# Kernel tuning notes

Measured on AMD Instinct MI355X. Metric: run time of the kernel, lower is better.

Reference implementation:

```python
import jax, jax.numpy as jnp
import numpy as np

IN_CH = 512; OUT_CH = 512; NOISE_SIZE = 512; K = 3; A = 0.2
B = 4; H = 32
_G = float(np.sqrt(2.0 / (1.0 + A * A)))                 # leaky_relu gain, a=0.2
CONV_SCALE = _G / float(np.sqrt(IN_CH * K * K))          # equal-lr kaiming scale (fan_in = in_ch*3*3)
MS_SCALE = float(np.sqrt(2.0 / (NOISE_SIZE + IN_CH)))    # equal-lr xavier scale on make_s linear
RGB_SCALE = _G * float(np.sqrt(2.0 / (OUT_CH + 3)))      # equal-lr xavier scale on 1x1 to_rgb


def upsample2x(x):
    # torch F.interpolate(scale_factor=2, mode='bilinear', align_corners=False)
    b, c, h, w = x.shape
    return jax.image.resize(x, (b, c, 2 * h, 2 * w), method='bilinear')


def mod_conv(x, style, weight, bias, ms_w, ms_b, w_scale, demodulate, pad):
    # style -> per-sample input-channel scales s: (B, Cin)
    s = style @ (ms_w.T * MS_SCALE) + ms_b
    Wmod = (weight * w_scale)[None] * s[:, None, :, None, None]   # (B, Cout, Cin, k, k)
    if demodulate:
        d = jax.lax.rsqrt(jnp.sum(Wmod * Wmod, axis=(2, 3, 4)) + 1e-8)
        Wmod = Wmod * d[:, :, None, None, None]
    conv1 = lambda xi, wi: jax.lax.conv_general_dilated(
        xi[None], wi, (1, 1), [(pad, pad), (pad, pad)],
        dimension_numbers=('NCHW', 'OIHW', 'NCHW'))[0]
    y = jax.vmap(conv1)(x, Wmod)                                   # per-sample weights == grouped conv
    return y + bias[None, :, None, None]


def lrelu(x):
    return jnp.where(x >= 0, x, A * x)


def setup_inputs() -> dict:
    key = jax.random.key(0)
    ks = jax.random.split(key, 19)
    r = lambda i, shape: jax.random.normal(ks[i], shape, dtype=jnp.float32)
    return {
        'maps': r(0, (B, IN_CH, H, H)),
        'w': r(1, (B, NOISE_SIZE)),
        'rgb': r(2, (B, 3, H, H)),
        'noise0': r(3, (B, 1, 2 * H, 2 * H)),
        'noise1': r(4, (B, 1, 2 * H, 2 * H)),
        'conv0_w': r(5, (OUT_CH, IN_CH, K, K)),
        'conv0_b': 0.1 * r(6, (OUT_CH,)),
        'ms0_w': r(7, (IN_CH, NOISE_SIZE)),
        'ms0_b': jnp.ones((IN_CH,), jnp.float32),
        'ns0': 0.1 * r(8, (OUT_CH,)),
        'conv1_w': r(9, (OUT_CH, OUT_CH, K, K)),
        'conv1_b': 0.1 * r(10, (OUT_CH,)),
        'ms1_w': r(11, (OUT_CH, NOISE_SIZE)),
        'ms1_b': jnp.ones((OUT_CH,), jnp.float32),
        'ns1': 0.1 * r(12, (OUT_CH,)),
        'rgb_w': r(13, (3, OUT_CH, 1, 1)),
        'rgb_b': 0.1 * r(14, (3,)),
        'msr_w': r(15, (OUT_CH, NOISE_SIZE)),
        'msr_b': jnp.ones((OUT_CH,), jnp.float32),
    }


def reference(maps, w, rgb, noise0, noise1,
              conv0_w, conv0_b, ms0_w, ms0_b, ns0,
              conv1_w, conv1_b, ms1_w, ms1_b, ns1,
              rgb_w, rgb_b, msr_w, msr_b):
    # upsample branch (upsample=True)
    rgb = upsample2x(rgb)
    maps = upsample2x(maps)
    # layer 0: modulated conv -> noise -> leaky relu
    h = mod_conv(maps, w, conv0_w, conv0_b, ms0_w, ms0_b, CONV_SCALE, True, 1)
    h = lrelu(h + ns0[None, :, None, None] * noise0)
    # layer 1
    h = mod_conv(h, w, conv1_w, conv1_b, ms1_w, ms1_b, CONV_SCALE, True, 1)
    h = lrelu(h + ns1[None, :, None, None] * noise1)
    # to_rgb: 1x1 modulated conv, no demodulation
    rgb_out = rgb + mod_conv(h, w, rgb_w, rgb_b, msr_w, msr_b, RGB_SCALE, False, 0)
    return (rgb_out, h)
```

## Files before the change

### kernel.cpp

```cpp
#include <hip/hip_runtime.h>
#include <stdint.h>


#define BATCH 4
#define CH 512
#define NPP 4356
#define HOUT_OFF 49152

static constexpr double G_GAIN = 1.3867504905630728;
static constexpr float CONV_SCALE_F = (float)(G_GAIN / 67.88225099390857);
static constexpr float MS_SCALE_F = 0.044194173824159216f;
static constexpr float RGB_SCALE_F = (float)(G_GAIN * 1.4142135623730951 / 22.693611435820433);

typedef __attribute__((ext_vector_type(8))) short short8;
typedef __attribute__((ext_vector_type(4))) float floatx4;

#define OFF_S0     256
#define OFF_S1     (OFF_S0 + 8192)
#define OFF_SR     (OFF_S1 + 8192)
#define OFF_D0     (OFF_SR + 8192)
#define OFF_D1     (OFF_D0 + 8192)
#define OFF_B0F    (OFF_D1 + 8192)
#define OFF_B1F    (OFF_B0F + 2048)
#define OFF_NS0F   (OFF_B1F + 2048)
#define OFF_NS1F   (OFF_NS0F + 2048)
#define OFF_N0F    (OFF_NS1F + 2048)
#define OFF_N1F    (OFF_N0F + 65536)
#define OFF_WT0    (OFF_N1F + 65536)
#define WT_BYTES   4718592
#define OFF_WT1    (OFF_WT0 + WT_BYTES)
#define OFF_XP0    (OFF_WT1 + WT_BYTES)
#define XP_BYTES   17842176
#define OFF_XP1    (OFF_XP0 + XP_BYTES)

__device__ __forceinline__ float bf2f(unsigned short u) {
  return __uint_as_float(((unsigned int)u) << 16);
}
__device__ __forceinline__ unsigned short f2bf(float f) {
  unsigned int x = __float_as_uint(f);
  unsigned int r = x + 0x7FFFu + ((x >> 16) & 1u);
  return (unsigned short)(r >> 16);
}
__device__ __forceinline__ float ldin(const void* p, long i, int bf) {
  if (bf) return bf2f(((const unsigned short*)p)[i]);
  return ((const float*)p)[i];
}
__device__ __forceinline__ int bfflag_of(const void* msb) {
  return ((const unsigned int*)msb)[0] == 0x3F803F80u ? 1 : 0;
}
__device__ __forceinline__ void async_ld16(const void* g, void* l) {
  __builtin_amdgcn_global_load_lds(
      (const __attribute__((address_space(1))) unsigned int*)g,
      (__attribute__((address_space(3))) unsigned int*)l, 16, 0, 0);
}
__device__ __forceinline__ void upw(int o, int n_in, int& lo, int& hi, float& wlo) {
  int k = o >> 1;
  if (o & 1) { lo = k; hi = k + 1; if (hi > n_in - 1) hi = n_in - 1; wlo = 0.75f; }
  else       { lo = k - 1; if (lo < 0) lo = 0; hi = k; wlo = 0.25f; }
}

__global__ void k_pre(const void* w, const void* msw0, const void* msb0,
                      const void* msw1, const void* msb1,
                      const void* mswr, const void* msbr,
                      const void* b0, const void* b1, const void* nv0,
                      const void* nv1, const void* noise0, const void* noise1,
                      float* s0, float* s1, float* sr,
                      float* ob0, float* ob1, float* ons0, float* ons1,
                      float* on0, float* on1, unsigned short* Xp) {
  const int bf = bfflag_of(msb0);
  const int bid = blockIdx.x;
  if (bid < 264) {
    const int idx = bid * 256 + threadIdx.x;
    const int plane = idx / 132;
    const int rem = idx - plane * 132;
    const int row65 = rem >= 66;
    const int col = rem - (row65 ? 66 : 0);
    const short8 z = {0, 0, 0, 0, 0, 0, 0, 0};
    *(short8*)&Xp[((long)plane * NPP + (row65 ? 65 : 0) * 66 + col) * 8] = z;
    return;
  }
  if (bid < 648) {
    const int b2 = bid - 264;
    const int mat = b2 >> 7, chunk = b2 & 127;
    const int wv = threadIdx.x >> 6, lane = threadIdx.x & 63;
    const int i = chunk * 4 + wv;
    const void* msw; const void* msb; float* out;
    if (mat == 0)      { msw = msw0; msb = msb0; out = s0; }
    else if (mat == 1) { msw = msw1; msb = msb1; out = s1; }
    else               { msw = mswr; msb = msbr; out = sr; }
    float a[4] = {0.f, 0.f, 0.f, 0.f};
    const int n0 = lane * 8;
    if (bf) {
      short8 m8 = *(const short8*)((const unsigned short*)msw + (long)i * 512 + n0);
      for (int b = 0; b < 4; ++b) {
        short8 w8 = *(const short8*)((const unsigned short*)w + b * 512 + n0);
        float s = 0.f;
        for (int e = 0; e < 8; ++e)
          s += bf2f((unsigned short)m8[e]) * bf2f((unsigned short)w8[e]);
        a[b] = s;
      }
    } else {
      const float* mrow = (const float*)msw + (long)i * 512 + n0;
      float4 m0v = *(const float4*)mrow, m1v = *(const float4*)(mrow + 4);
      for (int b = 0; b < 4; ++b) {
        const float* wr = (const float*)w + b * 512 + n0;
        float4 w0v = *(const float4*)wr, w1v = *(const float4*)(wr + 4);
        a[b] = m0v.x * w0v.x + m0v.y * w0v.y + m0v.z * w0v.z + m0v.w * w0v.w +
               m1v.x * w1v.x + m1v.y * w1v.y + m1v.z * w1v.z + m1v.w * w1v.w;
      }
    }
    for (int off = 1; off < 64; off <<= 1)
      for (int b = 0; b < 4; ++b) a[b] += __shfl_xor(a[b], off, 64);
    if (lane == 0) {
      const float mb = ldin(msb, i, bf);
      for (int b = 0; b < 4; ++b) out[b * 512 + i] = a[b] * MS_SCALE_F + mb;
    }
    return;
  }
  const int t = (bid - 648) * 256 + threadIdx.x;
  if (t < 512) {
    ob0[t] = ldin(b0, t, bf); ob1[t] = ldin(b1, t, bf);
    ons0[t] = ldin(nv0, t, bf); ons1[t] = ldin(nv1, t, bf);
  }
  on0[t] = ldin(noise0, t, bf);
  on1[t] = ldin(noise1, t, bf);
}

__global__ void k_wtd(const void* w0, const void* w1, const float* s0, const float* s1,
                      unsigned short* Wt0, unsigned short* Wt1,
                      float* S0, float* S1, const void* msb) {
  const int bf = bfflag_of(msb);
  const int l = blockIdx.x >> 9, co = blockIdx.x & 511;
  const void* w = l ? w1 : w0;
  const float* s = l ? s1 : s0;
  unsigned short* Wt = l ? Wt1 : Wt0;
  float* S = l ? S1 : S0;
  float part[4] = {0.f, 0.f, 0.f, 0.f};
  for (int h = 0; h < 2; ++h) {
    const int ci = threadIdx.x + h * 256;
    const int kb = ci >> 5, q = (ci >> 3) & 3, j = ci & 7;
    const long rbase = ((long)co * 512 + ci) * 9;
    float wsq = 0.f;
    for (int t = 0; t < 9; ++t) {
      float v = ldin(w, rbase + t, bf);
      wsq += v * v;
      Wt[((((long)t * 16 + kb) * 4 + q) * 512 + co) * 8 + j] = f2bf(v);
    }
    for (int b = 0; b < 4; ++b) {
      float sv = s[b * 512 + ci];
      part[b] += sv * sv * wsq;
    }
  }
  __shared__ float red[256 * 4];
  for (int b = 0; b < 4; ++b) red[threadIdx.x * 4 + b] = part[b];
  __syncthreads();
  for (int off = 128; off > 0; off >>= 1) {
    if (threadIdx.x < off)
      for (int b = 0; b < 4; ++b)
        red[threadIdx.x * 4 + b] += red[(threadIdx.x + off) * 4 + b];
    __syncthreads();
  }
  if (threadIdx.x < 4) S[threadIdx.x * 512 + co] = red[threadIdx.x];
}

__global__ void k_upt(const void* maps, const float* s0, unsigned short* Xp0,
                      const void* msb) {
  const int bf = bfflag_of(msb);
  const int t = blockIdx.x, kb = blockIdx.y, b = blockIdx.z;
  __shared__ float lds[32][4][32];
  {
    const int ciq = threadIdx.x >> 5;
    const int x = threadIdx.x & 31;
    for (int cc = 0; cc < 4; ++cc) {
      const int ci = cc * 8 + ciq;
      const long cbase = ((long)(b * 512 + kb * 32 + ci)) << 10;
      for (int r = 0; r < 4; ++r) {
        int ir = 2 * t - 1 + r;
        ir = ir < 0 ? 0 : (ir > 31 ? 31 : ir);
        lds[ci][r][x] = ldin(maps, cbase + ir * 32 + x, bf);
      }
    }
  }
  __syncthreads();
  const int q = threadIdx.x >> 6, px = threadIdx.x & 63;
  int xlo, xhi; float wx;
  upw(px, 32, xlo, xhi, wx);
  float sv[8];
  for (int jj = 0; jj < 8; ++jj) sv[jj] = s0[b * 512 + kb * 32 + q * 8 + jj];
  for (int y = 0; y < 4; ++y) {
    const int yg = 4 * t + y;
    int ylo, yhi; float wy;
    upw(yg, 32, ylo, yhi, wy);
    const int rlo = ylo - (2 * t - 1), rhi = yhi - (2 * t - 1);
    short8 pk;
    for (int jj = 0; jj < 8; ++jj) {
      const int ci = q * 8 + jj;
      float vlo = wx * lds[ci][rlo][xlo] + (1.f - wx) * lds[ci][rlo][xhi];
      float vhi = wx * lds[ci][rhi][xlo] + (1.f - wx) * lds[ci][rhi][xhi];
      float v = (wy * vlo + (1.f - wy) * vhi) * sv[jj];
      pk[jj] = (short)f2bf(v);
    }
    *(short8*)&Xp0[((((long)b * 16 + kb) * 4 + q) * NPP + (yg + 1) * 66 + (px + 1)) * 8] = pk;
  }
}

#define MFMA16 __builtin_amdgcn_mfma_f32_16x16x32_bf16
template <int LAYER>
__global__ __launch_bounds__(256, 2) void k_conv(
    const unsigned short* __restrict__ Wt,
    const unsigned short* Xp,
    const float* __restrict__ Ssum,
    const float* __restrict__ bias,
    const float* __restrict__ nsc,
    const float* __restrict__ noise,
    const float* __restrict__ snext,
    unsigned short* XpOut,
    void* dout,
    const void* __restrict__ msb) {
  __shared__ __align__(16) unsigned short AB[32768];
  const int idx = blockIdx.x;
  const int mt = idx & 3, b = (idx >> 2) & 3, nt = idx >> 4;
  const int m0 = mt << 7, y0 = nt << 1;
  const int lane = threadIdx.x & 63, wv = threadIdx.x >> 6;
  const int wm = wv >> 1, wn = wv & 1;
  const int q = lane >> 4, l15 = lane & 15;

  const floatx4 vz = {0.f, 0.f, 0.f, 0.f};
  floatx4 c00 = vz, c01 = vz, c02 = vz, c03 = vz;
  floatx4 c10 = vz, c11 = vz, c12 = vz, c13 = vz;
  floatx4 c20 = vz, c21 = vz, c22 = vz, c23 = vz;
  floatx4 c30 = vz, c31 = vz, c32 = vz, c33 = vz;

  const int vA = (q << 10) + (wm << 9) + (l15 << 3);
  const int BB = 24576;
  const int vB   = BB + (q << 9) + (l15 << 3);
  const int vBm1 = BB + (q << 9) + ((l15 == 0 ? 0 : l15 - 1) << 3);
  const int vBp1 = BB + (q << 9) + ((l15 == 15 ? 15 : l15 + 1) << 3);
  const bool e0 = (l15 == 0), e15 = (l15 == 15);
  const int c6 = wv * 6;

  auto issueB2 = [&](int kb, int r0) {
    for (int r = 0; r < 2; ++r) {
      const int row = r0 + r;
      const unsigned short* src =
          Xp + ((((long)b * 16 + kb) * 4 + wv) * NPP + (long)(y0 + row) * 66 + 1 + lane) * 8;
      async_ld16(src, &AB[BB + ((row * 4 + wv) << 9)]);
    }
  };
  auto issueA = [&](int kb, int ky, int par) {
#pragma unroll
    for (int k = 0; k < 6; ++k) {
      const int c = c6 + k;
      const int half = c & 1, chunk = c >> 1;
      const int kx = chunk >> 2, qq = chunk & 3;
      const unsigned short* src =
          Wt + ((long)(((ky * 3 + kx) * 16 + kb) * 4 + qq) << 12) +
          ((m0 + half * 64 + lane) << 3);
      async_ld16(src, &AB[par * 12288 + chunk * 1024 + half * 512]);
    }
  };

  const short8 z8 = {0, 0, 0, 0, 0, 0, 0, 0};

#define RND(KY, PA, KB, NKB, NKY, NPA, DOB, DKB, DR0)                          \
  {                                                                            \
    __syncthreads();                                                           \
    issueA((NKB), (NKY), (NPA));                                               \
    if (DOB) issueB2((DKB), (DR0));                                            \
    const int ab = (PA) * 12288 + vA;                                          \
    short8 a00 = *(const short8*)&AB[ab];                                      \
    short8 a01 = *(const short8*)&AB[ab + 128];                                \
    short8 a02 = *(const short8*)&AB[ab + 256];                                \
    short8 a03 = *(const short8*)&AB[ab + 384];                                \
    short8 a10 = *(const short8*)&AB[ab + 4096];                               \
    short8 a11 = *(const short8*)&AB[ab + 4224];                               \
    short8 a12 = *(const short8*)&AB[ab + 4352];                               \
    short8 a13 = *(const short8*)&AB[ab + 4480];                               \
    short8 a20 = *(const short8*)&AB[ab + 8192];                               \
    short8 a21 = *(const short8*)&AB[ab + 8320];                               \
    short8 a22 = *(const short8*)&AB[ab + 8448];                               \
    short8 a23 = *(const short8*)&AB[ab + 8576];                               \
    const int bo = ((wn + (KY)) << 11);                                        \
    {                                                              \
      short8 b0 = *(const short8*)&AB[vBm1 + bo];                              \
      short8 b1 = *(const short8*)&AB[vB + bo + 120];                          \
      short8 b2 = *(const short8*)&AB[vB + bo + 248];                          \
      short8 b3 = *(const short8*)&AB[vB + bo + 376];                          \
      b0 = e0 ? z8 : b0;                                                       \
      c00 = MFMA16(a00, b0, c00, 0, 0, 0); c01 = MFMA16(a00, b1, c01, 0, 0, 0);\
      c02 = MFMA16(a00, b2, c02, 0, 0, 0); c03 = MFMA16(a00, b3, c03, 0, 0, 0);\
      c10 = MFMA16(a01, b0, c10, 0, 0, 0); c11 = MFMA16(a01, b1, c11, 0, 0, 0);\
      c12 = MFMA16(a01, b2, c12, 0, 0, 0); c13 = MFMA16(a01, b3, c13, 0, 0, 0);\
      c20 = MFMA16(a02, b0, c20, 0, 0, 0); c21 = MFMA16(a02, b1, c21, 0, 0, 0);\
      c22 = MFMA16(a02, b2, c22, 0, 0, 0); c23 = MFMA16(a02, b3, c23, 0, 0, 0);\
      c30 = MFMA16(a03, b0, c30, 0, 0, 0); c31 = MFMA16(a03, b1, c31, 0, 0, 0);\
      c32 = MFMA16(a03, b2, c32, 0, 0, 0); c33 = MFMA16(a03, b3, c33, 0, 0, 0);\
    }                                                                          \
    {                                                              \
      short8 b0 = *(const short8*)&AB[vB + bo];                                \
      short8 b1 = *(const short8*)&AB[vB + bo + 128];                          \
      short8 b2 = *(const short8*)&AB[vB + bo + 256];                          \
      short8 b3 = *(const short8*)&AB[vB + bo + 384];                          \
      c00 = MFMA16(a10, b0, c00, 0, 0, 0); c01 = MFMA16(a10, b1, c01, 0, 0, 0);\
      c02 = MFMA16(a10, b2, c02, 0, 0, 0); c03 = MFMA16(a10, b3, c03, 0, 0, 0);\
      c10 = MFMA16(a11, b0, c10, 0, 0, 0); c11 = MFMA16(a11, b1, c11, 0, 0, 0);\
      c12 = MFMA16(a11, b2, c12, 0, 0, 0); c13 = MFMA16(a11, b3, c13, 0, 0, 0);\
      c20 = MFMA16(a12, b0, c20, 0, 0, 0); c21 = MFMA16(a12, b1, c21, 0, 0, 0);\
      c22 = MFMA16(a12, b2, c22, 0, 0, 0); c23 = MFMA16(a12, b3, c23, 0, 0, 0);\
      c30 = MFMA16(a13, b0, c30, 0, 0, 0); c31 = MFMA16(a13, b1, c31, 0, 0, 0);\
      c32 = MFMA16(a13, b2, c32, 0, 0, 0); c33 = MFMA16(a13, b3, c33, 0, 0, 0);\
    }                                                                          \
    {                                                              \
      short8 b0 = *(const short8*)&AB[vB + bo + 8];                            \
      short8 b1 = *(const short8*)&AB[vB + bo + 136];                          \
      short8 b2 = *(const short8*)&AB[vB + bo + 264];                          \
      short8 b3 = *(const short8*)&AB[vBp1 + bo + 384];                        \
      b3 = e15 ? z8 : b3;                                                      \
      c00 = MFMA16(a20, b0, c00, 0, 0, 0); c01 = MFMA16(a20, b1, c01, 0, 0, 0);\
      c02 = MFMA16(a20, b2, c02, 0, 0, 0); c03 = MFMA16(a20, b3, c03, 0, 0, 0);\
      c10 = MFMA16(a21, b0, c10, 0, 0, 0); c11 = MFMA16(a21, b1, c11, 0, 0, 0);\
      c12 = MFMA16(a21, b2, c12, 0, 0, 0); c13 = MFMA16(a21, b3, c13, 0, 0, 0);\
      c20 = MFMA16(a22, b0, c20, 0, 0, 0); c21 = MFMA16(a22, b1, c21, 0, 0, 0);\
      c22 = MFMA16(a22, b2, c22, 0, 0, 0); c23 = MFMA16(a22, b3, c23, 0, 0, 0);\
      c30 = MFMA16(a23, b0, c30, 0, 0, 0); c31 = MFMA16(a23, b1, c31, 0, 0, 0);\
      c32 = MFMA16(a23, b2, c32, 0, 0, 0); c33 = MFMA16(a23, b3, c33, 0, 0, 0);\
    }                                                                          \
  }

  issueA(0, 0, 0);
  issueB2(0, 0);

#pragma unroll 1
  for (int it = 0; it < 8; ++it) {
    const int kb = it * 2, kb1 = kb + 1, kb2 = (kb + 2) & 15;
    RND(0, 0, kb,  kb,  1, 1, 1, kb,  2)
    RND(1, 1, kb,  kb,  2, 0, 0, 0,  0)
    RND(2, 0, kb,  kb1, 0, 1, 1, kb1, 0)
    RND(0, 1, kb1, kb1, 1, 0, 1, kb1, 2)
    RND(1, 0, kb1, kb1, 2, 1, 0, 0,  0)
    RND(2, 1, kb1, kb2, 0, 0, 1, kb2, 0)
  }
#undef RND

  floatx4 accv[4][4] = {{c00, c01, c02, c03}, {c10, c11, c12, c13},
                        {c20, c21, c22, c23}, {c30, c31, c32, c33}};
  const int bfflag = bfflag_of(msb);
  const int coB = m0 + (wm << 6) + ((lane >> 4) << 2);
  const int xB = lane & 15;
  const int y = y0 + wn;
  for (int i = 0; i < 4; ++i) {
    const int co = coB + (i << 4);
    float Ds[4], bi[4], nv[4], sx[4];
    for (int r = 0; r < 4; ++r) {
      float Sv = Ssum[b * 512 + co + r];
      Ds[r] = CONV_SCALE_F * rsqrtf(CONV_SCALE_F * CONV_SCALE_F * Sv + 1e-8f);
      bi[r] = bias[co + r];
      nv[r] = nsc[co + r];
      sx[r] = (LAYER == 0) ? snext[b * 512 + co + r] : 0.f;
    }
    for (int j = 0; j < 4; ++j) {
      const int x = (j << 4) + xB;
      const int p = (y << 6) + x;
      const float nz = noise[b * 4096 + p];
      if (LAYER == 0) {
        unsigned long long pk = 0ull;
        for (int r = 0; r < 4; ++r) {
          float v = accv[i][j][r] * Ds[r] + bi[r] + nv[r] * nz;
          v = (v >= 0.f) ? v : 0.2f * v;
          pk |= (unsigned long long)f2bf(v * sx[r]) << (16 * r);
        }
        const int pp = (y + 1) * 66 + (x + 1);
        const long o = ((((long)b * 16 + (co >> 5)) * 4 + ((co >> 3) & 3)) * NPP + pp) * 8 + (co & 7);
        *(unsigned long long*)(XpOut + o) = pk;
      } else {
        for (int r = 0; r < 4; ++r) {
          float v = accv[i][j][r] * Ds[r] + bi[r] + nv[r] * nz;
          v = (v >= 0.f) ? v : 0.2f * v;
          const long o = (((long)(b * 512 + co + r)) << 12) + p;
          if (bfflag) ((unsigned short*)dout)[HOUT_OFF + o] = f2bf(v);
          else        ((float*)dout)[HOUT_OFF + o] = v;
        }
      }
    }
  }
}

__global__ void k_rgb(const void* rgb_in, const void* rw, const void* rb,
                      const float* sr, void* dout, const void* msb) {
  const int bf = bfflag_of(msb);
  const int b = blockIdx.y, p0 = blockIdx.x * 64;
  const int px = threadIdx.x & 63, g = threadIdx.x >> 6;
  const char* hbytes = (const char*)dout + (long)HOUT_OFF * (bf ? 2 : 4);
  const float* srb = sr + b * 512;
  float a0 = 0.f, a1 = 0.f, a2 = 0.f;
  for (int ci = g * 128; ci < g * 128 + 128; ++ci) {
    const long o = (((long)(b * 512 + ci)) << 12) + p0 + px;
    const float hv = bf ? bf2f(((const unsigned short*)hbytes)[o])
                        : ((const float*)hbytes)[o];
    const float sh = srb[ci] * hv;
    a0 += RGB_SCALE_F * ldin(rw, ci, bf) * sh;
    a1 += RGB_SCALE_F * ldin(rw, 512 + ci, bf) * sh;
    a2 += RGB_SCALE_F * ldin(rw, 1024 + ci, bf) * sh;
  }
  __shared__ float red[4][3][64];
  red[g][0][px] = a0; red[g][1][px] = a1; red[g][2][px] = a2;
  __syncthreads();
  if (g == 0) {
    const int p = p0 + px;
    const int y = p >> 6, x = p & 63;
    int ylo, yhi, xlo, xhi; float wy, wx;
    upw(y, 32, ylo, yhi, wy);
    upw(x, 32, xlo, xhi, wx);
    for (int c = 0; c < 3; ++c) {
      float s = red[0][c][px] + red[1][c][px] + red[2][c][px] + red[3][c][px];
      const long base = (long)(b * 3 + c) << 10;
      const float v00 = ldin(rgb_in, base + ylo * 32 + xlo, bf);
      const float v01 = ldin(rgb_in, base + ylo * 32 + xhi, bf);
      const float v10 = ldin(rgb_in, base + yhi * 32 + xlo, bf);
      const float v11 = ldin(rgb_in, base + yhi * 32 + xhi, bf);
      const float up = wy * (wx * v00 + (1.f - wx) * v01) +
                       (1.f - wy) * (wx * v10 + (1.f - wx) * v11);
      const float v = up + s + ldin(rb, c, bf);
      const long o = ((long)(b * 3 + c) << 12) + p;
      if (bf) ((unsigned short*)dout)[o] = f2bf(v);
      else    ((float*)dout)[o] = v;
    }
  }
}

extern "C" void kernel_launch(void* const* d_in, const int* in_sizes, int n_in,
                              void* d_out, int out_size, void* d_ws, size_t ws_size,
                              hipStream_t stream) {
  char* ws = (char*)d_ws;
  float* s0 = (float*)(ws + OFF_S0);
  float* s1 = (float*)(ws + OFF_S1);
  float* sr = (float*)(ws + OFF_SR);
  float* S0 = (float*)(ws + OFF_D0);
  float* S1 = (float*)(ws + OFF_D1);
  float* b0f = (float*)(ws + OFF_B0F);
  float* b1f = (float*)(ws + OFF_B1F);
  float* ns0f = (float*)(ws + OFF_NS0F);
  float* ns1f = (float*)(ws + OFF_NS1F);
  float* n0f = (float*)(ws + OFF_N0F);
  float* n1f = (float*)(ws + OFF_N1F);
  unsigned short* Wt0 = (unsigned short*)(ws + OFF_WT0);
  unsigned short* Wt1 = (unsigned short*)(ws + OFF_WT1);
  unsigned short* Xp0 = (unsigned short*)(ws + OFF_XP0);
  unsigned short* Xp1 = (unsigned short*)(ws + OFF_XP1);

  k_pre<<<712, 256, 0, stream>>>(d_in[1], d_in[7], d_in[8], d_in[12], d_in[13],
                                 d_in[17], d_in[18], d_in[6], d_in[11], d_in[9],
                                 d_in[14], d_in[3], d_in[4],
                                 s0, s1, sr, b0f, b1f, ns0f, ns1f, n0f, n1f, Xp0);
  k_wtd<<<1024, 256, 0, stream>>>(d_in[5], d_in[10], s0, s1, Wt0, Wt1, S0, S1,
                                  d_in[8]);
  k_upt<<<dim3(16, 16, 4), 256, 0, stream>>>(d_in[0], s0, Xp0, d_in[8]);
  k_conv<0><<<512, 256, 0, stream>>>(Wt0, Xp0, S0, b0f, ns0f, n0f, s1, Xp1,
                                     d_out, d_in[8]);
  k_conv<1><<<512, 256, 0, stream>>>(Wt1, Xp1, S1, b1f, ns1f, n1f, s1, Xp1,
                                     d_out, d_in[8]);
  k_rgb<<<dim3(64, 4), 256, 0, stream>>>(d_in[2], d_in[15], d_in[16], sr, d_out,
                                         d_in[8]);
  (void)in_sizes; (void)n_in; (void)out_size; (void)ws_size;
}
```

Measured before the change: 305.0 us.

## Fuse weight-transform and upsample kernels, vectorize weight prep, precompute to_rgb weights

Merges the weight transpose/demod-sum kernel and the upsample kernel into a single launch, which also precomputes the modulated to_rgb weights. The weight path now has each thread load 72 contiguous weights with vector loads, write packed short8 rows and reduce with wave shuffles instead of an LDS tree. k_rgb processes 8 pixels per thread with vector loads and reads the precomputed modulated weights. This cuts launch count and uncoalesced scalar traffic, but leaves k_rgb with only 32 blocks, which may underfill the GPU.

```diff
diff --git a/kernel.cpp b/kernel.cpp
--- a/kernel.cpp
+++ b/kernel.cpp
@@ -24,7 +24,8 @@
 #define OFF_B1F    (OFF_B0F + 2048)
 #define OFF_NS0F   (OFF_B1F + 2048)
 #define OFF_NS1F   (OFF_NS0F + 2048)
-#define OFF_N0F    (OFF_NS1F + 2048)
+#define OFF_WMODR  (OFF_NS1F + 2048)
+#define OFF_N0F    (OFF_WMODR + 24576)
 #define OFF_N1F    (OFF_N0F + 65536)
 #define OFF_WT0    (OFF_N1F + 65536)
 #define WT_BYTES   4718592
@@ -126,82 +127,131 @@
   on1[t] = ldin(noise1, t, bf);
 }
 
-__global__ void k_wtd(const void* w0, const void* w1, const float* s0, const float* s1,
-                      unsigned short* Wt0, unsigned short* Wt1,
-                      float* S0, float* S1, const void* msb) {
+__global__ void k_mid(const void* w0, const void* w1,
+                      const float* s0, const float* s1, const float* sr,
+                      const void* rw, unsigned short* Wt0, unsigned short* Wt1,
+                      float* S0, float* S1, float* owmr,
+                      const void* maps, unsigned short* Xp0, const void* msb) {
   const int bf = bfflag_of(msb);
-  const int l = blockIdx.x >> 9, co = blockIdx.x & 511;
-  const void* w = l ? w1 : w0;
-  const float* s = l ? s1 : s0;
-  unsigned short* Wt = l ? Wt1 : Wt0;
-  float* S = l ? S1 : S0;
-  float part[4] = {0.f, 0.f, 0.f, 0.f};
-  for (int h = 0; h < 2; ++h) {
-    const int ci = threadIdx.x + h * 256;
-    const int kb = ci >> 5, q = (ci >> 3) & 3, j = ci & 7;
-    const long rbase = ((long)co * 512 + ci) * 9;
-    float wsq = 0.f;
+  const int bid = blockIdx.x;
+  __shared__ float smem[32 * 4 * 32];
+  if (bid < 256) {
+    const int l = bid >> 7, cog = bid & 127;
+    const void* w = l ? w1 : w0;
+    const float* s = l ? s1 : s0;
+    unsigned short* Wt = l ? Wt1 : Wt0;
+    float* S = l ? S1 : S0;
+    const int co_sub = threadIdx.x >> 6;
+    const int kb = (threadIdx.x >> 2) & 15, q = threadIdx.x & 3;
+    const int co = cog * 4 + co_sub;
+    const int ci0 = kb * 32 + q * 8;
+    const long base = ((long)co * 512 + ci0) * 9;
+    float v[9][8];
+    if (bf) {
+      const unsigned short* wp = (const unsigned short*)w + base;
+      short8 r[9];
+#pragma unroll
+      for (int k = 0; k < 9; ++k) r[k] = *(const short8*)(wp + k * 8);
+#pragma unroll
+      for (int j = 0; j < 8; ++j)
+#pragma unroll
+        for (int t = 0; t < 9; ++t) {
+          const int off = j * 9 + t;
+          v[t][j] = bf2f((unsigned short)r[off >> 3][off & 7]);
+        }
+    } else {
+      const float* wp = (const float*)w + base;
+      float4 r[18];
+#pragma unroll
+      for (int k = 0; k < 18; ++k) r[k] = *(const float4*)(wp + k * 4);
+#pragma unroll
+      for (int j = 0; j < 8; ++j)
+#pragma unroll
+        for (int t = 0; t < 9; ++t) {
+          const int off = j * 9 + t;
+          const float4 rr = r[off >> 2];
+          const int c2 = off & 3;
+          v[t][j] = c2 == 0 ? rr.x : (c2 == 1 ? rr.y : (c2 == 2 ? rr.z : rr.w));
+        }
+    }
+#pragma unroll
     for (int t = 0; t < 9; ++t) {
-      float v = ldin(w, rbase + t, bf);
-      wsq += v * v;
-      Wt[((((long)t * 16 + kb) * 4 + q) * 512 + co) * 8 + j] = f2bf(v);
-    }
-    for (int b = 0; b < 4; ++b) {
-      float sv = s[b * 512 + ci];
-      part[b] += sv * sv * wsq;
-    }
-  }
-  __shared__ float red[256 * 4];
-  for (int b = 0; b < 4; ++b) red[threadIdx.x * 4 + b] = part[b];
-  __syncthreads();
-  for (int off = 128; off > 0; off >>= 1) {
-    if (threadIdx.x < off)
-      for (int b = 0; b < 4; ++b)
-        red[threadIdx.x * 4 + b] += red[(threadIdx.x + off) * 4 + b];
+      short8 pk;
+#pragma unroll
+      for (int j = 0; j < 8; ++j) pk[j] = (short)f2bf(v[t][j]);
+      *(short8*)&Wt[((long)(t * 16 + kb) * 4 + q) * 4096 + co * 8] = pk;
+    }
+    float wsq[8];
+#pragma unroll
+    for (int j = 0; j < 8; ++j) {
+      float a = 0.f;
+#pragma unroll
+      for (int t = 0; t < 9; ++t) a += v[t][j] * v[t][j];
+      wsq[j] = a;
+    }
+    float part[4];
+#pragma unroll
+    for (int b4 = 0; b4 < 4; ++b4) {
+      const float* sp = s + b4 * 512 + ci0;
+      float4 sa = *(const float4*)sp, sb = *(const float4*)(sp + 4);
+      part[b4] = sa.x * sa.x * wsq[0] + sa.y * sa.y * wsq[1] +
+                 sa.z * sa.z * wsq[2] + sa.w * sa.w * wsq[3] +
+                 sb.x * sb.x * wsq[4] + sb.y * sb.y * wsq[5] +
+                 sb.z * sb.z * wsq[6] + sb.w * sb.w * wsq[7];
+    }
+    for (int off = 1; off < 64; off <<= 1)
+#pragma unroll
+      for (int b4 = 0; b4 < 4; ++b4)
+        part[b4] += __shfl_xor(part[b4], off, 64);
+    if ((threadIdx.x & 63) == 0)
+#pragma unroll
+      for (int b4 = 0; b4 < 4; ++b4) S[b4 * 512 + co] = part[b4];
+    return;
+  }
+  if (bid < 1280) {
+    const int bid2 = bid - 256;
+    const int t = bid2 & 15, kb = (bid2 >> 4) & 15, b = bid2 >> 8;
+    float (*lds)[4][32] = (float(*)[4][32])smem;
+    {
+      const int ciq = threadIdx.x >> 5;
+      const int x = threadIdx.x & 31;
+      for (int cc = 0; cc < 4; ++cc) {
+        const int ci = cc * 8 + ciq;
+        const long cbase = ((long)(b * 512 + kb * 32 + ci)) << 10;
+        for (int r = 0; r < 4; ++r) {
+          int ir = 2 * t - 1 + r;
+          ir = ir < 0 ? 0 : (ir > 31 ? 31 : ir);
+          lds[ci][r][x] = ldin(maps, cbase + ir * 32 + x, bf);
+        }
+      }
+    }
     __syncthreads();
-  }
-  if (threadIdx.x < 4) S[threadIdx.x * 512 + co] = red[threadIdx.x];
-}
-
-__global__ void k_upt(const void* maps, const float* s0, unsigned short* Xp0,
-                      const void* msb) {
-  const int bf = bfflag_of(msb);
-  const int t = blockIdx.x, kb = blockIdx.y, b = blockIdx.z;
-  __shared__ float lds[32][4][32];
-  {
-    const int ciq = threadIdx.x >> 5;
-    const int x = threadIdx.x & 31;
-    for (int cc = 0; cc < 4; ++cc) {
-      const int ci = cc * 8 + ciq;
-      const long cbase = ((long)(b * 512 + kb * 32 + ci)) << 10;
-      for (int r = 0; r < 4; ++r) {
-        int ir = 2 * t - 1 + r;
-        ir = ir < 0 ? 0 : (ir > 31 ? 31 : ir);
-        lds[ci][r][x] = ldin(maps, cbase + ir * 32 + x, bf);
+    const int q = threadIdx.x >> 6, px = threadIdx.x & 63;
+    int xlo, xhi; float wx;
+    upw(px, 32, xlo, xhi, wx);
+    float sv[8];
+    for (int jj = 0; jj < 8; ++jj) sv[jj] = s0[b * 512 + kb * 32 + q * 8 + jj];
+    for (int y = 0; y < 4; ++y) {
+      const int yg = 4 * t + y;
+      int ylo, yhi; float wy;
+      upw(yg, 32, ylo, yhi, wy);
+      const int rlo = ylo - (2 * t - 1), rhi = yhi - (2 * t - 1);
+      short8 pk;
+      for (int jj = 0; jj < 8; ++jj) {
+        const int ci = q * 8 + jj;
+        float vlo = wx * lds[ci][rlo][xlo] + (1.f - wx) * lds[ci][rlo][xhi];
+        float vhi = wx * lds[ci][rhi][xlo] + (1.f - wx) * lds[ci][rhi][xhi];
+        float v = (wy * vlo + (1.f - wy) * vhi) * sv[jj];
+        pk[jj] = (short)f2bf(v);
       }
-    }
-  }
-  __syncthreads();
-  const int q = threadIdx.x >> 6, px = threadIdx.x & 63;
-  int xlo, xhi; float wx;
-  upw(px, 32, xlo, xhi, wx);
-  float sv[8];
-  for (int jj = 0; jj < 8; ++jj) sv[jj] = s0[b * 512 + kb * 32 + q * 8 + jj];
-  for (int y = 0; y < 4; ++y) {
-    const int yg = 4 * t + y;
-    int ylo, yhi; float wy;
-    upw(yg, 32, ylo, yhi, wy);
-    const int rlo = ylo - (2 * t - 1), rhi = yhi - (2 * t - 1);
-    short8 pk;
-    for (int jj = 0; jj < 8; ++jj) {
-      const int ci = q * 8 + jj;
-      float vlo = wx * lds[ci][rlo][xlo] + (1.f - wx) * lds[ci][rlo][xhi];
-      float vhi = wx * lds[ci][rhi][xlo] + (1.f - wx) * lds[ci][rhi][xhi];
-      float v = (wy * vlo + (1.f - wy) * vhi) * sv[jj];
-      pk[jj] = (short)f2bf(v);
-    }
-    *(short8*)&Xp0[((((long)b * 16 + kb) * 4 + q) * NPP + (yg + 1) * 66 + (px + 1)) * 8] = pk;
-  }
+      *(short8*)&Xp0[((((long)b * 16 + kb) * 4 + q) * NPP + (yg + 1) * 66 + (px + 1)) * 8] = pk;
+    }
+    return;
+  }
+  const int i = (bid - 1280) * 256 + threadIdx.x;
+  const int b = i / 1536; const int r = i - b * 1536;
+  const int c = r >> 9; const int ci = r & 511;
+  owmr[i] = RGB_SCALE_F * ldin(rw, c * 512 + ci, bf) * sr[b * 512 + ci];
 }
 
 #define MFMA16 __builtin_amdgcn_mfma_f32_16x16x32_bf16
@@ -385,34 +435,51 @@
   }
 }
 
-__global__ void k_rgb(const void* rgb_in, const void* rw, const void* rb,
-                      const float* sr, void* dout, const void* msb) {
+__global__ void k_rgb(const void* rgb_in, const float* wmodr, const void* rb,
+                      void* dout, const void* msb) {
   const int bf = bfflag_of(msb);
-  const int b = blockIdx.y, p0 = blockIdx.x * 64;
-  const int px = threadIdx.x & 63, g = threadIdx.x >> 6;
+  const int b = blockIdx.y, p0 = blockIdx.x * 512;
+  const int g = threadIdx.x >> 6, lane = threadIdx.x & 63;
+  const int px = p0 + lane * 8;
   const char* hbytes = (const char*)dout + (long)HOUT_OFF * (bf ? 2 : 4);
-  const float* srb = sr + b * 512;
-  float a0 = 0.f, a1 = 0.f, a2 = 0.f;
+  const float* wm = wmodr + b * 1536;
+  float a0[8] = {}, a1[8] = {}, a2[8] = {};
   for (int ci = g * 128; ci < g * 128 + 128; ++ci) {
-    const long o = (((long)(b * 512 + ci)) << 12) + p0 + px;
-    const float hv = bf ? bf2f(((const unsigned short*)hbytes)[o])
-                        : ((const float*)hbytes)[o];
-    const float sh = srb[ci] * hv;
-    a0 += RGB_SCALE_F * ldin(rw, ci, bf) * sh;
-    a1 += RGB_SCALE_F * ldin(rw, 512 + ci, bf) * sh;
-    a2 += RGB_SCALE_F * ldin(rw, 1024 + ci, bf) * sh;
-  }
-  __shared__ float red[4][3][64];
-  red[g][0][px] = a0; red[g][1][px] = a1; red[g][2][px] = a2;
+    const long o = (((long)(b * 512 + ci)) << 12) + px;
+    float hv[8];
+    if (bf) {
+      short8 h8 = *(const short8*)((const unsigned short*)hbytes + o);
+#pragma unroll
+      for (int k = 0; k < 8; ++k) hv[k] = bf2f((unsigned short)h8[k]);
+    } else {
+      float4 f0 = *(const float4*)((const float*)hbytes + o);
+      float4 f1 = *(const float4*)((const float*)hbytes + o + 4);
+      hv[0] = f0.x; hv[1] = f0.y; hv[2] = f0.z; hv[3] = f0.w;
+      hv[4] = f1.x; hv[5] = f1.y; hv[6] = f1.z; hv[7] = f1.w;
+    }
+    const float w0 = wm[ci], w1 = wm[512 + ci], w2 = wm[1024 + ci];
+#pragma unroll
+    for (int k = 0; k < 8; ++k) {
+      a0[k] += w0 * hv[k]; a1[k] += w1 * hv[k]; a2[k] += w2 * hv[k];
+    }
+  }
+  __shared__ float red[4][3][512];
+#pragma unroll
+  for (int k = 0; k < 8; ++k) {
+    red[g][0][lane * 8 + k] = a0[k];
+    red[g][1][lane * 8 + k] = a1[k];
+    red[g][2][lane * 8 + k] = a2[k];
+  }
   __syncthreads();
-  if (g == 0) {
-    const int p = p0 + px;
+  for (int e = 0; e < 2; ++e) {
+    const int pp = threadIdx.x * 2 + e;
+    const int p = p0 + pp;
     const int y = p >> 6, x = p & 63;
     int ylo, yhi, xlo, xhi; float wy, wx;
     upw(y, 32, ylo, yhi, wy);
     upw(x, 32, xlo, xhi, wx);
     for (int c = 0; c < 3; ++c) {
-      float s = red[0][c][px] + red[1][c][px] + red[2][c][px] + red[3][c][px];
+      float s = red[0][c][pp] + red[1][c][pp] + red[2][c][pp] + red[3][c][pp];
       const long base = (long)(b * 3 + c) << 10;
       const float v00 = ldin(rgb_in, base + ylo * 32 + xlo, bf);
       const float v01 = ldin(rgb_in, base + ylo * 32 + xhi, bf);
@@ -441,6 +508,7 @@
   float* b1f = (float*)(ws + OFF_B1F);
   float* ns0f = (float*)(ws + OFF_NS0F);
   float* ns1f = (float*)(ws + OFF_NS1F);
+  float* wmodr = (float*)(ws + OFF_WMODR);
   float* n0f = (float*)(ws + OFF_N0F);
   float* n1f = (float*)(ws + OFF_N1F);
   unsigned short* Wt0 = (unsigned short*)(ws + OFF_WT0);
@@ -452,14 +520,12 @@
                                  d_in[17], d_in[18], d_in[6], d_in[11], d_in[9],
                                  d_in[14], d_in[3], d_in[4],
                                  s0, s1, sr, b0f, b1f, ns0f, ns1f, n0f, n1f, Xp0);
-  k_wtd<<<1024, 256, 0, stream>>>(d_in[5], d_in[10], s0, s1, Wt0, Wt1, S0, S1,
-                                  d_in[8]);
-  k_upt<<<dim3(16, 16, 4), 256, 0, stream>>>(d_in[0], s0, Xp0, d_in[8]);
+  k_mid<<<1304, 256, 0, stream>>>(d_in[5], d_in[10], s0, s1, sr, d_in[15],
+                                  Wt0, Wt1, S0, S1, wmodr, d_in[0], Xp0, d_in[8]);
   k_conv<0><<<512, 256, 0, stream>>>(Wt0, Xp0, S0, b0f, ns0f, n0f, s1, Xp1,
                                      d_out, d_in[8]);
   k_conv<1><<<512, 256, 0, stream>>>(Wt1, Xp1, S1, b1f, ns1f, n1f, s1, Xp1,
                                      d_out, d_in[8]);
-  k_rgb<<<dim3(64, 4), 256, 0, stream>>>(d_in[2], d_in[15], d_in[16], sr, d_out,
-                                         d_in[8]);
+  k_rgb<<<dim3(8, 4), 256, 0, stream>>>(d_in[2], wmodr, d_in[16], d_out, d_in[8]);
   (void)in_sizes; (void)n_in; (void)out_size; (void)ws_size;
 }
```

Measured after the change: 293.7 us. -3.7%, faster.
